# Kernel optimization log

Measured on AMD Instinct MI355X. Metric: run time of the kernel, lower is better.

The kernel has to match this reference:

```python
import jax, jax.numpy as jnp
import numpy as np

D_K = 1024
NHEADS = 16
HEAD_DIM = D_K // NHEADS  # 64
STD = float(np.sqrt(HEAD_DIM))  # matches math.sqrt(d_k // nheads)


def setup_inputs() -> dict:
    key = jax.random.key(0)
    ks = jax.random.split(key, 9)
    B, S = 2, 2048
    scale = 1.0 / np.sqrt(D_K)
    x = jax.random.normal(ks[0], (B, S, D_K), dtype=jnp.float32)
    Wq = jax.random.normal(ks[1], (D_K, D_K), dtype=jnp.float32) * scale
    bq = jnp.zeros((D_K,), dtype=jnp.float32)
    Wk = jax.random.normal(ks[2], (D_K, D_K), dtype=jnp.float32) * scale
    bk = jnp.zeros((D_K,), dtype=jnp.float32)
    Wv = jax.random.normal(ks[3], (D_K, D_K), dtype=jnp.float32) * scale
    bv = jnp.zeros((D_K,), dtype=jnp.float32)
    Wo = jax.random.normal(ks[4], (D_K, D_K), dtype=jnp.float32) * scale
    bo = jnp.zeros((D_K,), dtype=jnp.float32)
    return {"x": x, "Wq": Wq, "bq": bq, "Wk": Wk, "bk": bk,
            "Wv": Wv, "bv": bv, "Wo": Wo, "bo": bo}


def _heads(x, W, b):
    # Linear then split heads: (B,S,D) -> (B,H,S,hd)
    B, S, _ = x.shape
    out = x @ W.T + b
    return out.reshape(B, S, NHEADS, HEAD_DIM).transpose(0, 2, 1, 3)


def reference(x, Wq, bq, Wk, bk, Wv, bv, Wo, bo):
    B, S, _ = x.shape
    q = _heads(x, Wq, bq)  # (B,H,S,hd)
    k = _heads(x, Wk, bk)
    v = _heads(x, Wv, bv)
    scores = jnp.einsum('bhqd,bhkd->bhqk', q, k) / STD  # (B,H,S,S)
    causal = jnp.tril(jnp.ones((S, S), dtype=bool))  # mask_factory default
    scores = jnp.where(causal[None, None, :, :], scores, -jnp.inf)
    attn = jax.nn.softmax(scores, axis=-1)
    ctx = jnp.einsum('bhqk,bhkd->bhqd', attn, v)  # (B,H,S,hd)
    ctx = ctx.transpose(0, 2, 1, 3).reshape(B, S, D_K)
    return ctx @ Wo.T + bo
```

## Files before the change

### kernel.cpp

```cpp
#include <hip/hip_runtime.h>
#include <stdint.h>

typedef unsigned short u16;
typedef __bf16 bf16x8 __attribute__((ext_vector_type(8)));
typedef __bf16 bf16x4v __attribute__((ext_vector_type(4)));
typedef float f32x4 __attribute__((ext_vector_type(4)));

typedef __attribute__((address_space(3))) uint32_t lds_u32;
typedef __attribute__((address_space(1))) uint32_t glb_u32;

__device__ __forceinline__ f32x4 mfma16(bf16x8 a, bf16x8 b, f32x4 c) {
    return __builtin_amdgcn_mfma_f32_16x16x32_bf16(a, b, c, 0, 0, 0);
}

__device__ __forceinline__ u16 f2b(float f) {
    union { float f; unsigned u32; } v; v.f = f;
    unsigned b = v.u32;
    unsigned r = b + 0x7FFFu + ((b >> 16) & 1u);
    return (u16)(r >> 16);
}

__device__ __forceinline__ ushort4 pk4(float a, float b, float c, float d) {
    bf16x4v v;
    v[0] = (__bf16)a; v[1] = (__bf16)b; v[2] = (__bf16)c; v[3] = (__bf16)d;
    union { bf16x4v v; ushort4 u; } cv; cv.v = v; return cv.u;
}

__device__ __forceinline__ void async16(const u16* g, u16* l) {
    __builtin_amdgcn_global_load_lds((glb_u32*)(uintptr_t)(const void*)g,
                                     (lds_u32*)l, 16, 0, 0);
}

__global__ __launch_bounds__(256) void cast_all(
    const float* __restrict__ x,
    const float* __restrict__ w0, const float* __restrict__ w1,
    const float* __restrict__ w2, const float* __restrict__ w3,
    u16* __restrict__ xo, u16* __restrict__ o0, u16* __restrict__ o1,
    u16* __restrict__ o2, u16* __restrict__ o3)
{
    const int s = blockIdx.y;
    const int i = (blockIdx.x * 256 + threadIdx.x) * 4;
    if (s == 0) {
#pragma unroll
        for (int c = 0; c < 4; ++c) {
            const int j = i + c * (1 << 20);
            float4 v = *(const float4*)(x + j);
            *(ushort4*)(xo + j) = pk4(v.x, v.y, v.z, v.w);
        }
    } else {
        const float* in = s == 1 ? w0 : (s == 2 ? w1 : (s == 3 ? w2 : w3));
        u16* out       = s == 1 ? o0 : (s == 2 ? o1 : (s == 3 ? o2 : o3));
        float4 v = *(const float4*)(in + i);
        *(ushort4*)(out + i) = pk4(v.x, v.y, v.z, v.w);
    }
}

__global__ __launch_bounds__(256) void gemm_qkv(
    const u16* __restrict__ A,
    const u16* __restrict__ W0, const u16* __restrict__ W1, const u16* __restrict__ W2,
    const float* __restrict__ B0, const float* __restrict__ B1, const float* __restrict__ B2,
    u16* __restrict__ O0, u16* __restrict__ O1,
    u16* __restrict__ VT,
    int M, int N, int K)
{
    const int sel = blockIdx.y;
    const u16* W      = sel == 0 ? W0 : (sel == 1 ? W1 : W2);
    const float* bias = sel == 0 ? B0 : (sel == 1 ? B1 : B2);
    u16* O            = sel == 0 ? O0 : O1;

    __shared__ __attribute__((aligned(16))) u16 As[128 * 32];
    __shared__ __attribute__((aligned(16))) u16 Bs[128 * 32];
    __shared__ __attribute__((aligned(16))) u16 Tb[32][136];

    const int tid  = threadIdx.x;
    const int lane = tid & 63;
    const int w    = tid >> 6;
    const int l15  = lane & 15;
    const int quad = lane >> 4;

    const int tn = (blockIdx.x & 7) << 7;
    const int tm = (blockIdx.x >> 3) << 7;
    const int wm = (w >> 1) << 6;
    const int wn = (w & 1) << 6;

    f32x4 acc[4][4];
#pragma unroll
    for (int i = 0; i < 4; ++i)
#pragma unroll
        for (int j = 0; j < 4; ++j) acc[i][j] = f32x4{0.f, 0.f, 0.f, 0.f};

    const int lr = lane >> 2;
    const int lc = (lane & 3) << 3;
    const u16* Ag0 = A + (size_t)(tm + 32 * w + lr) * K + lc;
    const u16* Ag1 = Ag0 + (size_t)16 * K;
    const u16* Wg0 = W + (size_t)(tn + 32 * w + lr) * K + lc;
    const u16* Wg1 = Wg0 + (size_t)16 * K;
    u16* Al0 = &As[(32 * w + lr) * 32 + lc];
    u16* Al1 = &As[(32 * w + 16 + lr) * 32 + lc];
    u16* Bl0 = &Bs[(32 * w + lr) * 32 + lc];
    u16* Bl1 = &Bs[(32 * w + 16 + lr) * 32 + lc];

    for (int k0 = 0; k0 < K; k0 += 32) {
        __syncthreads();
        async16(Ag0 + k0, Al0);
        async16(Ag1 + k0, Al1);
        async16(Wg0 + k0, Bl0);
        async16(Wg1 + k0, Bl1);
        asm volatile("s_waitcnt vmcnt(0)" ::: "memory");
        __syncthreads();

        bf16x8 a[4], b[4];
#pragma unroll
        for (int i = 0; i < 4; ++i)
            a[i] = *(const bf16x8*)&As[(wm + 16 * i + l15) * 32 + quad * 8];
#pragma unroll
        for (int j = 0; j < 4; ++j)
            b[j] = *(const bf16x8*)&Bs[(wn + 16 * j + l15) * 32 + quad * 8];
#pragma unroll
        for (int i = 0; i < 4; ++i)
#pragma unroll
            for (int j = 0; j < 4; ++j)
                acc[i][j] = mfma16(a[i], b[j], acc[i][j]);
    }

    if (sel == 2) {
        const int bb = tm >> 11;
        const int s0 = tm & 2047;
        const size_t vtb = ((size_t)bb << 10) + tn;
        for (int c32 = 0; c32 < 128; c32 += 32) {
            __syncthreads();
            if ((c32 >> 6) == (wn >> 6)) {
                const int j0 = (c32 >> 4) & 2;
#pragma unroll
                for (int jj = 0; jj < 2; ++jj) {
                    const int j  = j0 + jj;
                    const int cc = jj * 16 + l15;
                    const float bj = bias[tn + wn + 16 * j + l15];
#pragma unroll
                    for (int i = 0; i < 4; ++i) {
                        const int rr = wm + 16 * i + quad * 4;
                        *(ushort4*)&Tb[cc][rr] =
                            pk4(acc[i][j][0] + bj, acc[i][j][1] + bj,
                                acc[i][j][2] + bj, acc[i][j][3] + bj);
                    }
                }
            }
            __syncthreads();
            {
                const int c  = tid >> 3;
                const int ss = (tid & 7) * 16;
                uint4 v0 = *(const uint4*)&Tb[c][ss];
                uint4 v1 = *(const uint4*)&Tb[c][ss + 8];
                u16* dst = &VT[(vtb + c32 + c) * 2048 + s0 + ss];
                *(uint4*)dst       = v0;
                *(uint4*)(dst + 8) = v1;
            }
        }
    } else {
#pragma unroll
        for (int j = 0; j < 4; ++j) {
            const int col = tn + wn + 16 * j + l15;
            const float bj = bias[col];
#pragma unroll
            for (int i = 0; i < 4; ++i) {
                const int row = tm + wm + 16 * i + quad * 4;
#pragma unroll
                for (int r = 0; r < 4; ++r)
                    O[(size_t)(row + r) * N + col] = f2b(acc[i][j][r] + bj);
            }
        }
    }
}

__global__ __launch_bounds__(256) void gemm_out64(
    const u16* __restrict__ A, const u16* __restrict__ W,
    const float* __restrict__ bias, float* __restrict__ O,
    int M, int N, int K)
{
    __shared__ __attribute__((aligned(16))) u16 As[128 * 32];
    __shared__ __attribute__((aligned(16))) u16 Bs[64 * 32];

    const int tid  = threadIdx.x;
    const int lane = tid & 63;
    const int w    = tid >> 6;
    const int l15  = lane & 15;
    const int quad = lane >> 4;

    const int tn = (blockIdx.x & 15) << 6;
    const int tm = (blockIdx.x >> 4) << 7;
    const int wm = (w >> 1) << 6;
    const int wn = (w & 1) << 5;

    f32x4 acc[4][2];
#pragma unroll
    for (int i = 0; i < 4; ++i)
#pragma unroll
        for (int j = 0; j < 2; ++j) acc[i][j] = f32x4{0.f, 0.f, 0.f, 0.f};

    const int lr = lane >> 2;
    const int lc = (lane & 3) << 3;
    const u16* Ag0 = A + (size_t)(tm + 32 * w + lr) * K + lc;
    const u16* Ag1 = Ag0 + (size_t)16 * K;
    const u16* Wg  = W + (size_t)(tn + 16 * w + lr) * K + lc;
    u16* Al0 = &As[(32 * w + lr) * 32 + lc];
    u16* Al1 = &As[(32 * w + 16 + lr) * 32 + lc];
    u16* Bl  = &Bs[(16 * w + lr) * 32 + lc];

    for (int k0 = 0; k0 < K; k0 += 32) {
        __syncthreads();
        async16(Ag0 + k0, Al0);
        async16(Ag1 + k0, Al1);
        async16(Wg + k0, Bl);
        asm volatile("s_waitcnt vmcnt(0)" ::: "memory");
        __syncthreads();

        bf16x8 a[4], b[2];
#pragma unroll
        for (int i = 0; i < 4; ++i)
            a[i] = *(const bf16x8*)&As[(wm + 16 * i + l15) * 32 + quad * 8];
#pragma unroll
        for (int j = 0; j < 2; ++j)
            b[j] = *(const bf16x8*)&Bs[(wn + 16 * j + l15) * 32 + quad * 8];
#pragma unroll
        for (int i = 0; i < 4; ++i)
#pragma unroll
            for (int j = 0; j < 2; ++j)
                acc[i][j] = mfma16(a[i], b[j], acc[i][j]);
    }

#pragma unroll
    for (int j = 0; j < 2; ++j) {
        const int col = tn + wn + 16 * j + l15;
        const float bj = bias[col];
#pragma unroll
        for (int i = 0; i < 4; ++i) {
            const int row = tm + wm + 16 * i + quad * 4;
#pragma unroll
            for (int r = 0; r < 4; ++r)
                O[(size_t)(row + r) * N + col] = acc[i][j][r] + bj;
        }
    }
}

__device__ __forceinline__ bf16x8 rdt(const u16* base, int t, int l15, int cc) {
    const int r = t * 16 + l15;
    const int c = (cc & 3) ^ (r & 3);
    return *(const bf16x8*)(base + (cc >> 2) * 2048 + r * 32 + c * 8);
}

__global__ __launch_bounds__(256) void attn6(
    const u16* __restrict__ Q, const u16* __restrict__ Kb,
    const u16* __restrict__ VT, u16* __restrict__ ctx)
{
    __shared__ __attribute__((aligned(16))) u16 Kt[2][4096];
    __shared__ __attribute__((aligned(16))) u16 Vt[2][4096];
    __shared__ __attribute__((aligned(16))) u16 Pt[4][32][72];

    const int tid  = threadIdx.x;
    const int lane = tid & 63;
    const int wid  = tid >> 6;
    const int l15  = lane & 15;
    const int quad = lane >> 4;

    const int hb = blockIdx.x & 31;
    const int h  = hb & 15, b = hb >> 4;
    const int ti = blockIdx.x >> 5;
    const int g  = (ti & 1) ? (15 - (ti >> 1)) : (ti >> 1);

    const int sL = 4 * g + wid, sH = 127 - sL;
    const int KL = g, KH = 31 - g;

    const size_t rowbase = (size_t)b * 2048;
    const int cbase = h * 64;
    const u16* kbase = Kb + rowbase * 1024 + cbase;
    const u16* vbase = VT + ((size_t)b * 1024 + cbase) * 2048;

    const int qgL = sL * 16 + l15, qgH = sH * 16 + l15;
    const u16* qpL = Q + (rowbase + qgL) * 1024 + cbase + quad * 8;
    const u16* qpH = Q + (rowbase + qgH) * 1024 + cbase + quad * 8;
    const bf16x8 qL0 = *(const bf16x8*)qpL, qL1 = *(const bf16x8*)(qpL + 32);
    const bf16x8 qH0 = *(const bf16x8*)qpH, qH1 = *(const bf16x8*)(qpH + 32);

    const int sr  = tid >> 2;
    const int sc0 = (((tid & 3) ^ (sr & 3)) << 3);
    const u16* kg = kbase + (size_t)sr * 1024 + sc0;
    const u16* vg = vbase + (size_t)sr * 2048 + sc0;

    f32x4 oL[4], oH[4];
#pragma unroll
    for (int i = 0; i < 4; ++i) { oL[i] = f32x4{0,0,0,0}; oH[i] = f32x4{0,0,0,0}; }
    float rsL = 0.f, rsH = 0.f;
    const float SC = 0.18033688011112042f;

    u16 (*ptw)[72] = Pt[wid];

    async16(kg,      &Kt[0][tid * 8]);
    async16(kg + 32, &Kt[0][2048 + tid * 8]);
    async16(vg,      &Vt[0][tid * 8]);
    async16(vg + 32, &Vt[0][2048 + tid * 8]);

    for (int kt = 0; kt <= KH; ++kt) {
        const int cur = kt & 1, nxt = cur ^ 1;
        asm volatile("s_waitcnt vmcnt(0)" ::: "memory");
        __syncthreads();
        if (kt < KH) {
            const u16* kgn = kg + (size_t)(kt + 1) * 65536;
            const u16* vgn = vg + (kt + 1) * 64;
            async16(kgn,      &Kt[nxt][tid * 8]);
            async16(kgn + 32, &Kt[nxt][2048 + tid * 8]);
            async16(vgn,      &Vt[nxt][tid * 8]);
            async16(vgn + 32, &Vt[nxt][2048 + tid * 8]);
        }
        const u16* KT = Kt[cur];
        const u16* VL = Vt[cur];
        const bool doL = (kt <= KL);
        const bool mH = (kt == KH), mL = (kt == KL);

        float pH[4][4], pL[4][4];
#pragma unroll
        for (int t = 0; t < 4; ++t) {
            const bf16x8 kA = rdt(KT, t, l15, quad);
            const bf16x8 kB = rdt(KT, t, l15, quad + 4);
            f32x4 zH = {0,0,0,0};
            zH = mfma16(kA, qH0, zH);
            zH = mfma16(kB, qH1, zH);
            f32x4 zL = {0,0,0,0};
            if (doL) {
                zL = mfma16(kA, qL0, zL);
                zL = mfma16(kB, qL1, zL);
            }
#pragma unroll
            for (int r = 0; r < 4; ++r) {
                float v = fmaf(zH[r], SC, -16.0f);
                if (mH && (kt * 64 + t * 16 + quad * 4 + r) > qgH) v = -1e30f;
                const float e = exp2f(v);
                pH[t][r] = e; rsH += e;
                if (doL) {
                    float vl = fmaf(zL[r], SC, -16.0f);
                    if (mL && (kt * 64 + t * 16 + quad * 4 + r) > qgL) vl = -1e30f;
                    const float el = exp2f(vl);
                    pL[t][r] = el; rsL += el;
                }
            }
        }

#pragma unroll
        for (int t = 0; t < 4; ++t)
            *(ushort4*)&ptw[16 + l15][t * 16 + quad * 4] =
                pk4(pH[t][0], pH[t][1], pH[t][2], pH[t][3]);
        if (doL) {
#pragma unroll
            for (int t = 0; t < 4; ++t)
                *(ushort4*)&ptw[l15][t * 16 + quad * 4] =
                    pk4(pL[t][0], pL[t][1], pL[t][2], pL[t][3]);
        }

        const bf16x8 bH0 = *(const bf16x8*)&ptw[16 + l15][quad * 8];
        const bf16x8 bH1 = *(const bf16x8*)&ptw[16 + l15][32 + quad * 8];
#pragma unroll
        for (int t = 0; t < 4; ++t) {
            const bf16x8 vA = rdt(VL, t, l15, quad);
            const bf16x8 vB = rdt(VL, t, l15, quad + 4);
            oH[t] = mfma16(vA, bH0, oH[t]);
            oH[t] = mfma16(vB, bH1, oH[t]);
        }
        if (doL) {
            const bf16x8 bL0 = *(const bf16x8*)&ptw[l15][quad * 8];
            const bf16x8 bL1 = *(const bf16x8*)&ptw[l15][32 + quad * 8];
#pragma unroll
            for (int t = 0; t < 4; ++t) {
                const bf16x8 vA = rdt(VL, t, l15, quad);
                const bf16x8 vB = rdt(VL, t, l15, quad + 4);
                oL[t] = mfma16(vA, bL0, oL[t]);
                oL[t] = mfma16(vB, bL1, oL[t]);
            }
        }
    }

    rsH += __shfl_xor(rsH, 16); rsH += __shfl_xor(rsH, 32);
    rsL += __shfl_xor(rsL, 16); rsL += __shfl_xor(rsL, 32);
    const float iH = 1.0f / rsH, iL = 1.0f / rsL;
#pragma unroll
    for (int t = 0; t < 4; ++t) {
        *(ushort4*)&ctx[(rowbase + qgL) * 1024 + cbase + t * 16 + quad * 4] =
            pk4(oL[t][0] * iL, oL[t][1] * iL, oL[t][2] * iL, oL[t][3] * iL);
        *(ushort4*)&ctx[(rowbase + qgH) * 1024 + cbase + t * 16 + quad * 4] =
            pk4(oH[t][0] * iH, oH[t][1] * iH, oH[t][2] * iH, oH[t][3] * iH);
    }
}

extern "C" void kernel_launch(void* const* d_in, const int* in_sizes, int n_in,
                              void* d_out, int out_size, void* d_ws, size_t ws_size,
                              hipStream_t stream) {
    const float* x  = (const float*)d_in[0];
    const float* Wq = (const float*)d_in[1];
    const float* bq = (const float*)d_in[2];
    const float* Wk = (const float*)d_in[3];
    const float* bk = (const float*)d_in[4];
    const float* Wv = (const float*)d_in[5];
    const float* bv = (const float*)d_in[6];
    const float* Wo = (const float*)d_in[7];
    const float* bo = (const float*)d_in[8];
    float* out = (float*)d_out;

    const int N = 1024, K = 1024;
    const int M = in_sizes[0] / K;
    const size_t MN = (size_t)M * N;
    const size_t WN = (size_t)N * K;

    u16* xb  = (u16*)d_ws;
    u16* wqb = xb  + MN;
    u16* wkb = wqb + WN;
    u16* wvb = wkb + WN;
    u16* wob = wvb + WN;
    u16* q   = wob + WN;
    u16* kb  = q   + MN;
    u16* vt  = kb  + MN;
    u16* ctx = q;

    cast_all<<<dim3(1024, 5), 256, 0, stream>>>(
        x, Wq, Wk, Wv, Wo, xb, wqb, wkb, wvb, wob);

    const int gemmBlocks = (M / 128) * (N / 128);

    gemm_qkv<<<dim3(gemmBlocks, 3), 256, 0, stream>>>(
        xb, wqb, wkb, wvb, bq, bk, bv, q, kb, vt, M, N, K);

    attn6<<<dim3(512), 256, 0, stream>>>(q, kb, vt, ctx);

    gemm_out64<<<dim3((M / 128) * (N / 64)), 256, 0, stream>>>(
        ctx, wob, bo, out, M, N, K);
}
```

Baseline: 219.6 us.

## Double GEMM K-tile with XOR-swizzled LDS and XCD-aware block remapping

Both the QKV and output GEMMs now load 64-wide K tiles per iteration instead of 32. The LDS layout uses an XOR swizzle so the wider rows avoid bank conflicts. Block indices are remapped so that blocks on the same XCD (blockIdx mod 8) share nearby M/N tiles, which should improve L2 reuse. The transpose buffer now aliases As to keep the LDS footprint down, and grid sizes are hardcoded for M=4096, at the cost of flexibility.

Result: faster. 202.8 us (-7.7%).

```diff
diff --git a/kernel.cpp b/kernel.cpp
--- a/kernel.cpp
+++ b/kernel.cpp
@@ -11,13 +11,6 @@
 
 __device__ __forceinline__ f32x4 mfma16(bf16x8 a, bf16x8 b, f32x4 c) {
     return __builtin_amdgcn_mfma_f32_16x16x32_bf16(a, b, c, 0, 0, 0);
-}
-
-__device__ __forceinline__ u16 f2b(float f) {
-    union { float f; unsigned u32; } v; v.f = f;
-    unsigned b = v.u32;
-    unsigned r = b + 0x7FFFu + ((b >> 16) & 1u);
-    return (u16)(r >> 16);
 }
 
 __device__ __forceinline__ ushort4 pk4(float a, float b, float c, float d) {
@@ -63,14 +56,20 @@
     u16* __restrict__ VT,
     int M, int N, int K)
 {
-    const int sel = blockIdx.y;
+    const int x = blockIdx.x & 7;
+    const int L = blockIdx.x >> 3;
+    const int tm = (8 * (x >> 1) + (L & 7)) << 7;
+    const int tnsel = 12 * (x & 1) + (L >> 3);
+    const int sel = tnsel >> 3;
+    const int tn  = (tnsel & 7) << 7;
+
     const u16* W      = sel == 0 ? W0 : (sel == 1 ? W1 : W2);
     const float* bias = sel == 0 ? B0 : (sel == 1 ? B1 : B2);
     u16* O            = sel == 0 ? O0 : O1;
 
-    __shared__ __attribute__((aligned(16))) u16 As[128 * 32];
-    __shared__ __attribute__((aligned(16))) u16 Bs[128 * 32];
-    __shared__ __attribute__((aligned(16))) u16 Tb[32][136];
+    __shared__ __attribute__((aligned(16))) u16 As[128 * 64];
+    __shared__ __attribute__((aligned(16))) u16 Bs[128 * 64];
+    u16 (*Tb)[136] = (u16 (*)[136])As;
 
     const int tid  = threadIdx.x;
     const int lane = tid & 63;
@@ -78,8 +77,6 @@
     const int l15  = lane & 15;
     const int quad = lane >> 4;
 
-    const int tn = (blockIdx.x & 7) << 7;
-    const int tm = (blockIdx.x >> 3) << 7;
     const int wm = (w >> 1) << 6;
     const int wn = (w & 1) << 6;
 
@@ -89,38 +86,45 @@
 #pragma unroll
         for (int j = 0; j < 4; ++j) acc[i][j] = f32x4{0.f, 0.f, 0.f, 0.f};
 
-    const int lr = lane >> 2;
-    const int lc = (lane & 3) << 3;
-    const u16* Ag0 = A + (size_t)(tm + 32 * w + lr) * K + lc;
-    const u16* Ag1 = Ag0 + (size_t)16 * K;
-    const u16* Wg0 = W + (size_t)(tn + 32 * w + lr) * K + lc;
-    const u16* Wg1 = Wg0 + (size_t)16 * K;
-    u16* Al0 = &As[(32 * w + lr) * 32 + lc];
-    u16* Al1 = &As[(32 * w + 16 + lr) * 32 + lc];
-    u16* Bl0 = &Bs[(32 * w + lr) * 32 + lc];
-    u16* Bl1 = &Bs[(32 * w + 16 + lr) * 32 + lc];
-
-    for (int k0 = 0; k0 < K; k0 += 32) {
+    const int lr  = lane >> 3;
+    const int lcc = lane & 7;
+    const int scc = lcc ^ lr;
+    const u16* Ag = A + (size_t)(tm + 32 * w + lr) * K + scc * 8;
+    const u16* Wg = W + (size_t)(tn + 32 * w + lr) * K + scc * 8;
+    u16* Al = &As[(32 * w + lr) * 64 + lcc * 8];
+    u16* Bl = &Bs[(32 * w + lr) * 64 + lcc * 8];
+
+    for (int k0 = 0; k0 < K; k0 += 64) {
         __syncthreads();
-        async16(Ag0 + k0, Al0);
-        async16(Ag1 + k0, Al1);
-        async16(Wg0 + k0, Bl0);
-        async16(Wg1 + k0, Bl1);
+#pragma unroll
+        for (int m = 0; m < 4; ++m) {
+            async16(Ag + k0 + (size_t)m * 8 * K, Al + m * 512);
+            async16(Wg + k0 + (size_t)m * 8 * K, Bl + m * 512);
+        }
         asm volatile("s_waitcnt vmcnt(0)" ::: "memory");
         __syncthreads();
 
-        bf16x8 a[4], b[4];
-#pragma unroll
-        for (int i = 0; i < 4; ++i)
-            a[i] = *(const bf16x8*)&As[(wm + 16 * i + l15) * 32 + quad * 8];
-#pragma unroll
-        for (int j = 0; j < 4; ++j)
-            b[j] = *(const bf16x8*)&Bs[(wn + 16 * j + l15) * 32 + quad * 8];
-#pragma unroll
-        for (int i = 0; i < 4; ++i)
-#pragma unroll
-            for (int j = 0; j < 4; ++j)
-                acc[i][j] = mfma16(a[i], b[j], acc[i][j]);
+#pragma unroll
+        for (int kk = 0; kk < 2; ++kk) {
+            bf16x8 a[4], b[4];
+#pragma unroll
+            for (int i = 0; i < 4; ++i) {
+                const int r  = wm + 16 * i + l15;
+                const int sl = (kk * 4 + quad) ^ (r & 7);
+                a[i] = *(const bf16x8*)&As[r * 64 + sl * 8];
+            }
+#pragma unroll
+            for (int j = 0; j < 4; ++j) {
+                const int r  = wn + 16 * j + l15;
+                const int sl = (kk * 4 + quad) ^ (r & 7);
+                b[j] = *(const bf16x8*)&Bs[r * 64 + sl * 8];
+            }
+#pragma unroll
+            for (int i = 0; i < 4; ++i)
+#pragma unroll
+                for (int j = 0; j < 4; ++j)
+                    acc[i][j] = mfma16(a[i], b[j], acc[i][j]);
+        }
     }
 
     if (sel == 2) {
@@ -165,8 +169,11 @@
             for (int i = 0; i < 4; ++i) {
                 const int row = tm + wm + 16 * i + quad * 4;
 #pragma unroll
-                for (int r = 0; r < 4; ++r)
-                    O[(size_t)(row + r) * N + col] = f2b(acc[i][j][r] + bj);
+                for (int r = 0; r < 4; ++r) {
+                    union { float f; unsigned u; } v; v.f = acc[i][j][r] + bj;
+                    unsigned rn = v.u + 0x7FFFu + ((v.u >> 16) & 1u);
+                    O[(size_t)(row + r) * N + col] = (u16)(rn >> 16);
+                }
             }
         }
     }
@@ -177,8 +184,13 @@
     const float* __restrict__ bias, float* __restrict__ O,
     int M, int N, int K)
 {
-    __shared__ __attribute__((aligned(16))) u16 As[128 * 32];
-    __shared__ __attribute__((aligned(16))) u16 Bs[64 * 32];
+    __shared__ __attribute__((aligned(16))) u16 As[128 * 64];
+    __shared__ __attribute__((aligned(16))) u16 Bs[64 * 64];
+
+    const int x = blockIdx.x & 7;
+    const int L = blockIdx.x >> 3;
+    const int tm = (8 * (x >> 1) + (L & 7)) << 7;
+    const int tn = (8 * (x & 1) + (L >> 3)) << 6;
 
     const int tid  = threadIdx.x;
     const int lane = tid & 63;
@@ -186,8 +198,6 @@
     const int l15  = lane & 15;
     const int quad = lane >> 4;
 
-    const int tn = (blockIdx.x & 15) << 6;
-    const int tm = (blockIdx.x >> 4) << 7;
     const int wm = (w >> 1) << 6;
     const int wn = (w & 1) << 5;
 
@@ -197,35 +207,46 @@
 #pragma unroll
         for (int j = 0; j < 2; ++j) acc[i][j] = f32x4{0.f, 0.f, 0.f, 0.f};
 
-    const int lr = lane >> 2;
-    const int lc = (lane & 3) << 3;
-    const u16* Ag0 = A + (size_t)(tm + 32 * w + lr) * K + lc;
-    const u16* Ag1 = Ag0 + (size_t)16 * K;
-    const u16* Wg  = W + (size_t)(tn + 16 * w + lr) * K + lc;
-    u16* Al0 = &As[(32 * w + lr) * 32 + lc];
-    u16* Al1 = &As[(32 * w + 16 + lr) * 32 + lc];
-    u16* Bl  = &Bs[(16 * w + lr) * 32 + lc];
-
-    for (int k0 = 0; k0 < K; k0 += 32) {
+    const int lr  = lane >> 3;
+    const int lcc = lane & 7;
+    const int scc = lcc ^ lr;
+    const u16* Ag = A + (size_t)(tm + 32 * w + lr) * K + scc * 8;
+    const u16* Wg = W + (size_t)(tn + 16 * w + lr) * K + scc * 8;
+    u16* Al = &As[(32 * w + lr) * 64 + lcc * 8];
+    u16* Bl = &Bs[(16 * w + lr) * 64 + lcc * 8];
+
+    for (int k0 = 0; k0 < K; k0 += 64) {
         __syncthreads();
-        async16(Ag0 + k0, Al0);
-        async16(Ag1 + k0, Al1);
-        async16(Wg + k0, Bl);
+#pragma unroll
+        for (int m = 0; m < 4; ++m)
+            async16(Ag + k0 + (size_t)m * 8 * K, Al + m * 512);
+#pragma unroll
+        for (int m = 0; m < 2; ++m)
+            async16(Wg + k0 + (size_t)m * 8 * K, Bl + m * 512);
         asm volatile("s_waitcnt vmcnt(0)" ::: "memory");
         __syncthreads();
 
-        bf16x8 a[4], b[2];
-#pragma unroll
-        for (int i = 0; i < 4; ++i)
-            a[i] = *(const bf16x8*)&As[(wm + 16 * i + l15) * 32 + quad * 8];
-#pragma unroll
-        for (int j = 0; j < 2; ++j)
-            b[j] = *(const bf16x8*)&Bs[(wn + 16 * j + l15) * 32 + quad * 8];
-#pragma unroll
-        for (int i = 0; i < 4; ++i)
-#pragma unroll
-            for (int j = 0; j < 2; ++j)
-                acc[i][j] = mfma16(a[i], b[j], acc[i][j]);
+#pragma unroll
+        for (int kk = 0; kk < 2; ++kk) {
+            bf16x8 a[4], b[2];
+#pragma unroll
+            for (int i = 0; i < 4; ++i) {
+                const int r  = wm + 16 * i + l15;
+                const int sl = (kk * 4 + quad) ^ (r & 7);
+                a[i] = *(const bf16x8*)&As[r * 64 + sl * 8];
+            }
+#pragma unroll
+            for (int j = 0; j < 2; ++j) {
+                const int r  = wn + 16 * j + l15;
+                const int sl = (kk * 4 + quad) ^ (r & 7);
+                b[j] = *(const bf16x8*)&Bs[r * 64 + sl * 8];
+            }
+#pragma unroll
+            for (int i = 0; i < 4; ++i)
+#pragma unroll
+                for (int j = 0; j < 2; ++j)
+                    acc[i][j] = mfma16(a[i], b[j], acc[i][j]);
+        }
     }
 
 #pragma unroll
@@ -421,13 +442,11 @@
     cast_all<<<dim3(1024, 5), 256, 0, stream>>>(
         x, Wq, Wk, Wv, Wo, xb, wqb, wkb, wvb, wob);
 
-    const int gemmBlocks = (M / 128) * (N / 128);
-
-    gemm_qkv<<<dim3(gemmBlocks, 3), 256, 0, stream>>>(
+    gemm_qkv<<<dim3(768), 256, 0, stream>>>(
         xb, wqb, wkb, wvb, bq, bk, bv, q, kb, vt, M, N, K);
 
     attn6<<<dim3(512), 256, 0, stream>>>(q, kb, vt, ctx);
 
-    gemm_out64<<<dim3((M / 128) * (N / 64)), 256, 0, stream>>>(
+    gemm_out64<<<dim3(512), 256, 0, stream>>>(
         ctx, wob, bo, out, M, N, K);
 }
```
